# Optimization experiments

Measured on AMD Instinct MI355X. Metric: run time of the kernel, lower is better.

## Reference

```python
import jax, jax.numpy as jnp
import numpy as np

B, S, K, N, G = 2, 2048, 4096, 11008, 128  # tokens=B*S, group_size=G

def setup_inputs() -> dict:
    key = jax.random.key(0)
    k1, k2, k3, k4 = jax.random.split(key, 4)
    x = jax.random.normal(k1, (B, S, K), dtype=jnp.float16)
    # packed INT4 weights: one uint8 holds two nibbles along N (even col = low nibble)
    w_packed = jax.random.randint(k2, (K, N // 2), 0, 256, dtype=jnp.int32).astype(jnp.uint8)
    # realistic per-group scales (small positive) and integer zeros in [0,16)
    w_scale = (jax.random.uniform(k3, (K // G, N), dtype=jnp.float32) * 0.02 + 1e-3).astype(jnp.float16)
    w_zero = jax.random.randint(k4, (K // G, N), 0, 16).astype(jnp.float16)
    return {"x": x, "w_packed": w_packed, "w_scale": w_scale, "w_zero": w_zero}

def reference(x, w_packed, w_scale, w_zero):
    Kd, Nh = w_packed.shape  # [K, N//2]
    # unpack nibbles: even output column = low nibble, odd = high nibble
    low = (w_packed & 0xF).astype(jnp.float16)
    high = ((w_packed >> 4) & 0xF).astype(jnp.float16)
    w_int4 = jnp.stack([low, high], axis=-1).reshape(Kd, 2 * Nh)  # [K, N]
    # per-group dequant: group index = k // G along the K axis
    scale = jnp.repeat(w_scale, G, axis=0)  # [K, N]
    zero = jnp.repeat(w_zero, G, axis=0)    # [K, N]
    w = (w_int4 - zero) * scale             # fp16 dequantized weight [K, N]
    x2 = x.reshape(-1, Kd)                  # [M, K]
    # fp16 inputs, fp32 accumulation (matches tl.dot acc fp32), store fp16
    acc = jnp.einsum('mk,kn->mn', x2, w, preferred_element_type=jnp.float32)
    out = acc.astype(jnp.float16)
    return out.reshape(*x.shape[:-1], 2 * Nh)
```

## Files before the change

kernel.cpp:

```cpp
#include <hip/hip_runtime.h>
#include <hip/hip_bf16.h>
#include <stdint.h>

typedef __bf16 bf16_t;
typedef __bf16 bf16x8 __attribute__((ext_vector_type(8)));
typedef _Float16 f16;
typedef _Float16 f16x8 __attribute__((ext_vector_type(8)));
typedef _Float16 h2 __attribute__((ext_vector_type(2)));
typedef float floatx4 __attribute__((ext_vector_type(4)));
typedef uint32_t u32;

#define M_DIM 4096
#define K_DIM 4096
#define N_DIM 11008
#define GRP 128
#define NHALF (N_DIM / 2)
#define N64T (N_DIM / 64)
#define KTN (K_DIM / 64)
#define WB_DWORDS (N64T * KTN * 64 * 8)
#define WB_BYTES ((size_t)WB_DWORDS * 4)

__global__ __launch_bounds__(256) void repack_w_kernel(const int* __restrict__ wp,
                                                       u32* __restrict__ WB) {
  __shared__ unsigned char Wt[64][36];

  const u32 tid = threadIdx.x;
  const u32 n64 = blockIdx.x;
  const u32 kt  = blockIdx.y;

  {
    const u32 r = tid >> 2;
    const u32 c = (tid & 3u) * 8u;
    const int* src = wp + (size_t)(kt * 64u + r) * NHALF + n64 * 32u + c;
    int4 a = *(const int4*)(src);
    int4 b = *(const int4*)(src + 4);
    u32 lo = ((u32)a.x & 0xFFu) | (((u32)a.y & 0xFFu) << 8) |
             (((u32)a.z & 0xFFu) << 16) | (((u32)a.w & 0xFFu) << 24);
    u32 hi = ((u32)b.x & 0xFFu) | (((u32)b.y & 0xFFu) << 8) |
             (((u32)b.z & 0xFFu) << 16) | (((u32)b.w & 0xFFu) << 24);
    *(u32*)&Wt[r][c]      = lo;
    *(u32*)&Wt[r][c + 4u] = hi;
  }
  __syncthreads();

  const u32 tt    = tid & 3u;
  const u32 ks    = (tid >> 2) & 1u;
  const u32 lane0 = tid >> 3;
  const u32 l15   = lane0 & 15u;
  const u32 cb    = tt * 8u + (l15 >> 1);
  const u32 sh    = (l15 & 1u) * 4u;
  const size_t obase = ((size_t)(n64 * 64u + kt) * 64u) * 8u;

#pragma unroll
  for (int half = 0; half < 2; ++half) {
    const u32 lane = lane0 + (u32)half * 32u;
    const u32 kb   = ks * 32u + (lane >> 4) * 8u;
    u32 d = 0;
#pragma unroll
    for (int p = 0; p < 8; ++p) {
      const int j = (p < 4) ? (2 * p) : (2 * (p - 4) + 1);
      u32 byte = Wt[kb + (u32)j][cb];
      d |= ((byte >> sh) & 0xFu) << (4 * p);
    }
    WB[obase + tid + (u32)half * 256u] = d;
  }
}

__global__ __launch_bounds__(256) void gemm_int4_kernel(const float* __restrict__ x,
                                                        const u32* __restrict__ WB,
                                                        const float* __restrict__ wscale,
                                                        const float* __restrict__ wzero,
                                                        float* __restrict__ out) {
  __shared__ __align__(16) f16 As[128 * 64];

  const u32 tid  = threadIdx.x;
  const u32 lane = tid & 63u;
  const u32 wave = tid >> 6;
  const u32 l15  = lane & 15u;
  const u32 quad = lane >> 4;
  const u32 wr   = wave >> 1;
  const u32 wc   = wave & 1u;

  const u32 n0 = blockIdx.x * 128u;
  const u32 m0 = blockIdx.y * 128u;

  const u32 srow  = tid >> 3;
  const u32 sslot = tid & 7u;
  const float* xsrc = x + (size_t)(m0 + srow) * K_DIM + sslot * 8u;
  char* lds_dst = (char*)As + srow * 128u + ((sslot ^ (srow & 7u)) * 16u);

  const u32* wb_base = WB + ((size_t)((n0 >> 6) + wc) * KTN * 64u) * 8u + lane * 8u;

  const u32 arow = wr * 64u + l15;
  const f16* a0 = As + arow * 64u + (((quad)      ^ (l15 & 7u)) * 8u);
  const f16* a1 = As + arow * 64u + (((4u + quad) ^ (l15 & 7u)) * 8u);

  floatx4 acc[4][4];
  floatx4 zero4 = {0.f, 0.f, 0.f, 0.f};
#pragma unroll
  for (int i = 0; i < 4; ++i)
#pragma unroll
    for (int t = 0; t < 4; ++t) acc[i][t] = zero4;

  h2 s2[4], z2[4];
  const u32 nidx0 = n0 + wc * 64u + l15;

  for (u32 kt = 0; kt < KTN; ++kt) {
    const float* src = xsrc + kt * 64u;
    f16x8 av[4];
#pragma unroll
    for (int it = 0; it < 4; ++it) {
      float4 f0 = *(const float4*)(src + (size_t)it * 32 * K_DIM);
      float4 f1 = *(const float4*)(src + (size_t)it * 32 * K_DIM + 4);
      union { f16x8 v; h2 h[4]; } u;
      u.h[0] = __builtin_bit_cast(h2, __builtin_amdgcn_cvt_pkrtz(f0.x, f0.y));
      u.h[1] = __builtin_bit_cast(h2, __builtin_amdgcn_cvt_pkrtz(f0.z, f0.w));
      u.h[2] = __builtin_bit_cast(h2, __builtin_amdgcn_cvt_pkrtz(f1.x, f1.y));
      u.h[3] = __builtin_bit_cast(h2, __builtin_amdgcn_cvt_pkrtz(f1.z, f1.w));
      av[it] = u.v;
    }

    const u32* wp8 = wb_base + (size_t)kt * 512u;
    uint4 bq0 = *(const uint4*)(wp8);
    uint4 bq1 = *(const uint4*)(wp8 + 4u);

    if ((kt & 1u) == 0u) {
      const u32 g = kt >> 1;
#pragma unroll
      for (int t = 0; t < 4; ++t) {
        float s = wscale[g * N_DIM + nidx0 + (u32)t * 16u];
        float z = wzero [g * N_DIM + nidx0 + (u32)t * 16u];
        f16 sh_ = (f16)s;
        f16 zh_ = (f16)(1024.0f + z);
        h2 sv = {sh_, sh_};
        h2 zv = {zh_, zh_};
        s2[t] = sv;
        z2[t] = zv;
      }
    }

    __syncthreads();
#pragma unroll
    for (int it = 0; it < 4; ++it)
      *(f16x8*)(lds_dst + it * 4096) = av[it];
    __syncthreads();

#pragma unroll
    for (int ks = 0; ks < 2; ++ks) {
      f16x8 af[4];
      const f16* ab = ks ? a1 : a0;
#pragma unroll
      for (int i = 0; i < 4; ++i)
        af[i] = *(const f16x8*)(ab + i * 16 * 64);

      const uint4 bqv = ks ? bq1 : bq0;
      const u32 qs[4] = {bqv.x, bqv.y, bqv.z, bqv.w};
#pragma unroll
      for (int t = 0; t < 4; ++t) {
        const u32 q = qs[t];
        u32 w01 = (q & 0x000F000Fu) | 0x64006400u;
        u32 w23 = ((q >> 4) & 0x000F000Fu) | 0x64006400u;
        u32 w45 = ((q >> 8) & 0x000F000Fu) | 0x64006400u;
        u32 w67 = ((q >> 12) & 0x000F000Fu) | 0x64006400u;
        union { f16x8 v; h2 h[4]; } bf;
        bf.h[0] = (__builtin_bit_cast(h2, w01) - z2[t]) * s2[t];
        bf.h[1] = (__builtin_bit_cast(h2, w23) - z2[t]) * s2[t];
        bf.h[2] = (__builtin_bit_cast(h2, w45) - z2[t]) * s2[t];
        bf.h[3] = (__builtin_bit_cast(h2, w67) - z2[t]) * s2[t];
#pragma unroll
        for (int i = 0; i < 4; ++i)
          acc[i][t] = __builtin_amdgcn_mfma_f32_16x16x32_f16(af[i], bf.v, acc[i][t], 0, 0, 0);
      }
    }
  }

  const u32 col0 = n0 + wc * 64u + l15;
  const u32 row0 = m0 + wr * 64u + quad * 4u;
#pragma unroll
  for (int i = 0; i < 4; ++i)
#pragma unroll
    for (int t = 0; t < 4; ++t)
#pragma unroll
      for (int r = 0; r < 4; ++r)
        out[(size_t)(row0 + (u32)i * 16u + (u32)r) * N_DIM + col0 + (u32)t * 16u] =
            acc[i][t][r];
}

__global__ __launch_bounds__(256) void gemm_int4_direct(const float* __restrict__ x,
                                                        const int* __restrict__ wp,
                                                        const float* __restrict__ wscale,
                                                        const float* __restrict__ wzero,
                                                        float* __restrict__ out) {
  __shared__ __align__(16) bf16_t As[128 * 64];
  __shared__ unsigned char Wb[64 * 68];

  const u32 tid  = threadIdx.x;
  const u32 lane = tid & 63u;
  const u32 wave = tid >> 6;
  const u32 l15  = lane & 15u;
  const u32 quad = lane >> 4;

  const u32 n0 = blockIdx.x * 128u;
  const u32 m0 = blockIdx.y * 128u;

  const float* xsrc = x + (m0 + (tid >> 3)) * (u32)K_DIM + (tid & 7u) * 8u;
  char* lds_dst = (char*)(&As[0]) + tid * 16u;

  const u32 wrow = tid >> 2;
  const u32 wcol = (tid & 3u) * 16;
  const int* wsrc = wp + (size_t)wrow * NHALF + (n0 >> 1) + wcol;

  const u32 n_idx = n0 + wave * 32u + l15;
  const u32 bcol0 = (wave * 32u + l15) >> 1;
  const u32 bcol1 = (wave * 32u + 16u + l15) >> 1;
  const u32 nsh   = (l15 & 1u) * 4u;

  floatx4 acc[8][2];
  floatx4 zero4 = {0.f, 0.f, 0.f, 0.f};
#pragma unroll
  for (int i = 0; i < 8; ++i)
#pragma unroll
    for (int t = 0; t < 2; ++t) acc[i][t] = zero4;

  const bf16_t* afrag_base = &As[0] + l15 * 64u + quad * 8u;
  float sc[2], zs[2];

  for (u32 kt = 0; kt < K_DIM / 64u; ++kt) {
    const float* src = xsrc + kt * 64u;
    bf16x8 av[4];
#pragma unroll
    for (int it = 0; it < 4; ++it) {
      float4 f0 = *(const float4*)(src + it * 32 * K_DIM);
      float4 f1 = *(const float4*)(src + it * 32 * K_DIM + 4);
      bf16x8 v;
      v[0] = (bf16_t)f0.x; v[1] = (bf16_t)f0.y; v[2] = (bf16_t)f0.z; v[3] = (bf16_t)f0.w;
      v[4] = (bf16_t)f1.x; v[5] = (bf16_t)f1.y; v[6] = (bf16_t)f1.z; v[7] = (bf16_t)f1.w;
      av[it] = v;
    }

    const int* wsk = wsrc + (size_t)kt * 64u * NHALF;
    int4 wv[4];
#pragma unroll
    for (int q = 0; q < 4; ++q) wv[q] = *(const int4*)(wsk + q * 4);

    if ((kt & 1u) == 0u) {
      const u32 g = kt >> 1;
#pragma unroll
      for (int t = 0; t < 2; ++t) {
        float s = wscale[g * N_DIM + n_idx + t * 16u];
        float z = wzero[g * N_DIM + n_idx + t * 16u];
        sc[t] = s;
        zs[t] = s * z;
      }
    }

    __syncthreads();
#pragma unroll
    for (int it = 0; it < 4; ++it)
      *(bf16x8*)(lds_dst + it * 4096) = av[it];
#pragma unroll
    for (int q = 0; q < 4; ++q) {
      u32 d = ((u32)wv[q].x & 0xFFu) | (((u32)wv[q].y & 0xFFu) << 8) |
              (((u32)wv[q].z & 0xFFu) << 16) | (((u32)wv[q].w & 0xFFu) << 24);
      *(u32*)(&Wb[wrow * 68u + wcol + q * 4u]) = d;
    }
    __syncthreads();

#pragma unroll
    for (int ks = 0; ks < 2; ++ks) {
      bf16x8 af[8];
#pragma unroll
      for (int i = 0; i < 8; ++i)
        af[i] = *(const bf16x8*)(afrag_base + i * 16 * 64 + ks * 32);
#pragma unroll
      for (int t = 0; t < 2; ++t) {
        const u32 bc = t ? bcol1 : bcol0;
        bf16x8 bfr;
#pragma unroll
        for (int j = 0; j < 8; ++j) {
          u32 byte = Wb[(ks * 32u + quad * 8u + j) * 68u + bc];
          float w = (float)((byte >> nsh) & 0xFu) * sc[t] - zs[t];
          bfr[j] = (bf16_t)w;
        }
#pragma unroll
        for (int i = 0; i < 8; ++i)
          acc[i][t] = __builtin_amdgcn_mfma_f32_16x16x32_bf16(af[i], bfr, acc[i][t], 0, 0, 0);
      }
    }
  }

  const u32 col0 = n0 + wave * 32u + l15;
  const u32 row0 = m0 + quad * 4u;
#pragma unroll
  for (int i = 0; i < 8; ++i)
#pragma unroll
    for (int t = 0; t < 2; ++t)
#pragma unroll
      for (int r = 0; r < 4; ++r)
        out[(row0 + i * 16u + r) * (u32)N_DIM + col0 + t * 16u] = acc[i][t][r];
}

extern "C" void kernel_launch(void* const* d_in, const int* in_sizes, int n_in,
                              void* d_out, int out_size, void* d_ws, size_t ws_size,
                              hipStream_t stream) {
  const float* x      = (const float*)d_in[0];
  const int*   wp     = (const int*)d_in[1];
  const float* wscale = (const float*)d_in[2];
  const float* wzero  = (const float*)d_in[3];
  float*       out    = (float*)d_out;

  if (ws_size >= WB_BYTES && d_ws != nullptr) {
    u32* WB = (u32*)d_ws;
    repack_w_kernel<<<dim3(N64T, KTN), 256, 0, stream>>>(wp, WB);
    gemm_int4_kernel<<<dim3(N_DIM / 128, M_DIM / 128), 256, 0, stream>>>(x, WB, wscale, wzero, out);
  } else {
    gemm_int4_direct<<<dim3(N_DIM / 128, M_DIM / 128), 256, 0, stream>>>(x, wp, wscale, wzero, out);
  }
}
```

Measured before the change: 702.0 us.

## Double-buffer A tile in LDS, prefetch next tile, and remap workgroups per XCD

Restructures the GEMM main loop to use two LDS buffers for the A tile. Global loads of x, packed weights and scales for the next k-step are issued before the current tile's MFMA work, which cuts the loop to one barrier per step. It also launches a 1D grid and remaps block IDs so that each XCD gets a contiguous chunk of tiles sharing the same N column, aiming for better L2 reuse. In exchange the kernel uses twice the LDS and holds more registers for prefetched data, which may lower occupancy.

```diff
diff --git a/kernel.cpp b/kernel.cpp
--- a/kernel.cpp
+++ b/kernel.cpp
@@ -19,6 +19,8 @@
 #define KTN (K_DIM / 64)
 #define WB_DWORDS (N64T * KTN * 64 * 8)
 #define WB_BYTES ((size_t)WB_DWORDS * 4)
+#define NWG ((N_DIM / 128) * (M_DIM / 128))
+#define WG_PER_XCD (NWG / 8)
 
 __global__ __launch_bounds__(256) void repack_w_kernel(const int* __restrict__ wp,
                                                        u32* __restrict__ WB) {
@@ -66,12 +68,12 @@
   }
 }
 
-__global__ __launch_bounds__(256) void gemm_int4_kernel(const float* __restrict__ x,
-                                                        const u32* __restrict__ WB,
-                                                        const float* __restrict__ wscale,
-                                                        const float* __restrict__ wzero,
-                                                        float* __restrict__ out) {
-  __shared__ __align__(16) f16 As[128 * 64];
+__global__ __launch_bounds__(256) void gemm_int4_f16(const float* __restrict__ x,
+                                                     const u32* __restrict__ WB,
+                                                     const float* __restrict__ wscale,
+                                                     const float* __restrict__ wzero,
+                                                     float* __restrict__ out) {
+  __shared__ __align__(16) f16 As[2 * 128 * 64];
 
   const u32 tid  = threadIdx.x;
   const u32 lane = tid & 63u;
@@ -81,8 +83,10 @@
   const u32 wr   = wave >> 1;
   const u32 wc   = wave & 1u;
 
-  const u32 n0 = blockIdx.x * 128u;
-  const u32 m0 = blockIdx.y * 128u;
+  const u32 wgid = blockIdx.x;
+  const u32 gid  = (wgid & 7u) * WG_PER_XCD + (wgid >> 3);
+  const u32 n0   = (gid >> 5) * 128u;
+  const u32 m0   = (gid & 31u) * 128u;
 
   const u32 srow  = tid >> 3;
   const u32 sslot = tid & 7u;
@@ -91,9 +95,9 @@
 
   const u32* wb_base = WB + ((size_t)((n0 >> 6) + wc) * KTN * 64u) * 8u + lane * 8u;
 
-  const u32 arow = wr * 64u + l15;
-  const f16* a0 = As + arow * 64u + (((quad)      ^ (l15 & 7u)) * 8u);
-  const f16* a1 = As + arow * 64u + (((4u + quad) ^ (l15 & 7u)) * 8u);
+  const u32 abase = (wr * 64u + l15) * 64u;
+  const u32 sw0   = ((quad)      ^ (l15 & 7u)) * 8u;
+  const u32 sw1   = ((4u + quad) ^ (l15 & 7u)) * 8u;
 
   floatx4 acc[4][4];
   floatx4 zero4 = {0.f, 0.f, 0.f, 0.f};
@@ -102,58 +106,44 @@
 #pragma unroll
     for (int t = 0; t < 4; ++t) acc[i][t] = zero4;
 
-  h2 s2[4], z2[4];
   const u32 nidx0 = n0 + wc * 64u + l15;
 
-  for (u32 kt = 0; kt < KTN; ++kt) {
-    const float* src = xsrc + kt * 64u;
-    f16x8 av[4];
+  f16x8 nx[4];
+  auto loadx = [&](u32 kt) {
+    const float* p = xsrc + (size_t)kt * 64u;
 #pragma unroll
     for (int it = 0; it < 4; ++it) {
-      float4 f0 = *(const float4*)(src + (size_t)it * 32 * K_DIM);
-      float4 f1 = *(const float4*)(src + (size_t)it * 32 * K_DIM + 4);
+      float4 f0 = *(const float4*)(p + (size_t)it * 32 * K_DIM);
+      float4 f1 = *(const float4*)(p + (size_t)it * 32 * K_DIM + 4);
       union { f16x8 v; h2 h[4]; } u;
       u.h[0] = __builtin_bit_cast(h2, __builtin_amdgcn_cvt_pkrtz(f0.x, f0.y));
       u.h[1] = __builtin_bit_cast(h2, __builtin_amdgcn_cvt_pkrtz(f0.z, f0.w));
       u.h[2] = __builtin_bit_cast(h2, __builtin_amdgcn_cvt_pkrtz(f1.x, f1.y));
       u.h[3] = __builtin_bit_cast(h2, __builtin_amdgcn_cvt_pkrtz(f1.z, f1.w));
-      av[it] = u.v;
-    }
-
-    const u32* wp8 = wb_base + (size_t)kt * 512u;
-    uint4 bq0 = *(const uint4*)(wp8);
-    uint4 bq1 = *(const uint4*)(wp8 + 4u);
-
-    if ((kt & 1u) == 0u) {
-      const u32 g = kt >> 1;
-#pragma unroll
-      for (int t = 0; t < 4; ++t) {
-        float s = wscale[g * N_DIM + nidx0 + (u32)t * 16u];
-        float z = wzero [g * N_DIM + nidx0 + (u32)t * 16u];
-        f16 sh_ = (f16)s;
-        f16 zh_ = (f16)(1024.0f + z);
-        h2 sv = {sh_, sh_};
-        h2 zv = {zh_, zh_};
-        s2[t] = sv;
-        z2[t] = zv;
-      }
-    }
-
-    __syncthreads();
-#pragma unroll
-    for (int it = 0; it < 4; ++it)
-      *(f16x8*)(lds_dst + it * 4096) = av[it];
-    __syncthreads();
-
+      nx[it] = u.v;
+    }
+  };
+
+  loadx(0);
+  uint4 nbq0 = *(const uint4*)(wb_base);
+  uint4 nbq1 = *(const uint4*)(wb_base + 4u);
+  float fs[4], fz[4];
+#pragma unroll
+  for (int t = 0; t < 4; ++t) {
+    fs[t] = wscale[nidx0 + (u32)t * 16u];
+    fz[t] = wzero [nidx0 + (u32)t * 16u];
+  }
+  h2 s2[4], z2[4];
+
+  auto compute = [&](const f16* abuf, const uint4 bqa, const uint4 bqb) {
 #pragma unroll
     for (int ks = 0; ks < 2; ++ks) {
       f16x8 af[4];
-      const f16* ab = ks ? a1 : a0;
+      const f16* ab = abuf + abase + (ks ? sw1 : sw0);
 #pragma unroll
       for (int i = 0; i < 4; ++i)
         af[i] = *(const f16x8*)(ab + i * 16 * 64);
-
-      const uint4 bqv = ks ? bq1 : bq0;
+      const uint4 bqv = ks ? bqb : bqa;
       const u32 qs[4] = {bqv.x, bqv.y, bqv.z, bqv.w};
 #pragma unroll
       for (int t = 0; t < 4; ++t) {
@@ -172,6 +162,57 @@
           acc[i][t] = __builtin_amdgcn_mfma_f32_16x16x32_f16(af[i], bf.v, acc[i][t], 0, 0, 0);
       }
     }
+  };
+
+  for (u32 kt2 = 0; kt2 < KTN / 2; ++kt2) {
+#pragma unroll
+    for (int t = 0; t < 4; ++t) {
+      f16 sh_ = (f16)fs[t];
+      f16 zh_ = (f16)(1024.0f + fz[t]);
+      h2 sv = {sh_, sh_};
+      h2 zv = {zh_, zh_};
+      s2[t] = sv;
+      z2[t] = zv;
+    }
+    {
+      *(f16x8*)(lds_dst)         = nx[0];
+      *(f16x8*)(lds_dst + 4096)  = nx[1];
+      *(f16x8*)(lds_dst + 8192)  = nx[2];
+      *(f16x8*)(lds_dst + 12288) = nx[3];
+      uint4 cb0 = nbq0, cb1 = nbq1;
+      __syncthreads();
+      loadx(2u * kt2 + 1u);
+      {
+        const u32* wpn = wb_base + (size_t)(2u * kt2 + 1u) * 512u;
+        nbq0 = *(const uint4*)(wpn);
+        nbq1 = *(const uint4*)(wpn + 4u);
+      }
+      if (kt2 + 1u < (u32)(KTN / 2)) {
+        const u32 gofs = (kt2 + 1u) * (u32)N_DIM + nidx0;
+#pragma unroll
+        for (int t = 0; t < 4; ++t) {
+          fs[t] = wscale[gofs + (u32)t * 16u];
+          fz[t] = wzero [gofs + (u32)t * 16u];
+        }
+      }
+      compute(As, cb0, cb1);
+    }
+
+    {
+      *(f16x8*)(lds_dst + 16384)         = nx[0];
+      *(f16x8*)(lds_dst + 16384 + 4096)  = nx[1];
+      *(f16x8*)(lds_dst + 16384 + 8192)  = nx[2];
+      *(f16x8*)(lds_dst + 16384 + 12288) = nx[3];
+      uint4 cb0 = nbq0, cb1 = nbq1;
+      __syncthreads();
+      if (kt2 < (u32)(KTN / 2 - 1)) {
+        loadx(2u * kt2 + 2u);
+        const u32* wpn = wb_base + (size_t)(2u * kt2 + 2u) * 512u;
+        nbq0 = *(const uint4*)(wpn);
+        nbq1 = *(const uint4*)(wpn + 4u);
+      }
+      compute(As + 8192, cb0, cb1);
+    }
   }
 
   const u32 col0 = n0 + wc * 64u + l15;
@@ -312,7 +353,7 @@
   if (ws_size >= WB_BYTES && d_ws != nullptr) {
     u32* WB = (u32*)d_ws;
     repack_w_kernel<<<dim3(N64T, KTN), 256, 0, stream>>>(wp, WB);
-    gemm_int4_kernel<<<dim3(N_DIM / 128, M_DIM / 128), 256, 0, stream>>>(x, WB, wscale, wzero, out);
+    gemm_int4_f16<<<NWG, 256, 0, stream>>>(x, WB, wscale, wzero, out);
   } else {
     gemm_int4_direct<<<dim3(N_DIM / 128, M_DIM / 128), 256, 0, stream>>>(x, wp, wscale, wzero, out);
   }
```

Result: slower. 1.026 ms (+46.1%).

## Split waves along N so each wave covers all 128 rows and 32 columns

Applied to the files above, without the earlier changes.

The 128x128 block is now divided among its four waves along N only, so each wave computes a 128x32 output strip instead of a 64x64 quadrant. Each lane dequantizes two weight columns per k-step instead of four, which removes the duplicate dequantization that two waves previously did for the same columns. The cost is that every wave reads all eight A fragments from LDS per k-substep instead of four, which doubles LDS read traffic. Accumulator count and MFMA count per wave stay the same.

```diff
diff --git a/kernel.cpp b/kernel.cpp
--- a/kernel.cpp
+++ b/kernel.cpp
@@ -66,11 +66,11 @@
   }
 }
 
-__global__ __launch_bounds__(256) void gemm_int4_kernel(const float* __restrict__ x,
-                                                        const u32* __restrict__ WB,
-                                                        const float* __restrict__ wscale,
-                                                        const float* __restrict__ wzero,
-                                                        float* __restrict__ out) {
+__global__ __launch_bounds__(256) void gemm_int4_f16(const float* __restrict__ x,
+                                                     const u32* __restrict__ WB,
+                                                     const float* __restrict__ wscale,
+                                                     const float* __restrict__ wzero,
+                                                     float* __restrict__ out) {
   __shared__ __align__(16) f16 As[128 * 64];
 
   const u32 tid  = threadIdx.x;
@@ -78,8 +78,6 @@
   const u32 wave = tid >> 6;
   const u32 l15  = lane & 15u;
   const u32 quad = lane >> 4;
-  const u32 wr   = wave >> 1;
-  const u32 wc   = wave & 1u;
 
   const u32 n0 = blockIdx.x * 128u;
   const u32 m0 = blockIdx.y * 128u;
@@ -89,25 +87,27 @@
   const float* xsrc = x + (size_t)(m0 + srow) * K_DIM + sslot * 8u;
   char* lds_dst = (char*)As + srow * 128u + ((sslot ^ (srow & 7u)) * 16u);
 
-  const u32* wb_base = WB + ((size_t)((n0 >> 6) + wc) * KTN * 64u) * 8u + lane * 8u;
-
-  const u32 arow = wr * 64u + l15;
-  const f16* a0 = As + arow * 64u + (((quad)      ^ (l15 & 7u)) * 8u);
-  const f16* a1 = As + arow * 64u + (((4u + quad) ^ (l15 & 7u)) * 8u);
-
-  floatx4 acc[4][4];
+  const u32* wb_lane = WB + ((size_t)((n0 >> 6) + (wave >> 1)) * KTN * 512u)
+                         + lane * 8u + (wave & 1u) * 2u;
+
+  const u32 sw0 = ((quad)      ^ (l15 & 7u)) * 8u;
+  const u32 sw1 = ((4u + quad) ^ (l15 & 7u)) * 8u;
+  const f16* a0 = As + l15 * 64u + sw0;
+  const f16* a1 = As + l15 * 64u + sw1;
+
+  floatx4 acc[8][2];
   floatx4 zero4 = {0.f, 0.f, 0.f, 0.f};
 #pragma unroll
-  for (int i = 0; i < 4; ++i)
-#pragma unroll
-    for (int t = 0; t < 4; ++t) acc[i][t] = zero4;
-
-  h2 s2[4], z2[4];
-  const u32 nidx0 = n0 + wc * 64u + l15;
+  for (int i = 0; i < 8; ++i)
+#pragma unroll
+    for (int t = 0; t < 2; ++t) acc[i][t] = zero4;
+
+  const u32 nidx0 = n0 + wave * 32u + l15;
+  h2 s2[2], z2[2];
 
   for (u32 kt = 0; kt < KTN; ++kt) {
     const float* src = xsrc + kt * 64u;
-    f16x8 av[4];
+    f16x8 nx[4];
 #pragma unroll
     for (int it = 0; it < 4; ++it) {
       float4 f0 = *(const float4*)(src + (size_t)it * 32 * K_DIM);
@@ -117,17 +117,17 @@
       u.h[1] = __builtin_bit_cast(h2, __builtin_amdgcn_cvt_pkrtz(f0.z, f0.w));
       u.h[2] = __builtin_bit_cast(h2, __builtin_amdgcn_cvt_pkrtz(f1.x, f1.y));
       u.h[3] = __builtin_bit_cast(h2, __builtin_amdgcn_cvt_pkrtz(f1.z, f1.w));
-      av[it] = u.v;
-    }
-
-    const u32* wp8 = wb_base + (size_t)kt * 512u;
-    uint4 bq0 = *(const uint4*)(wp8);
-    uint4 bq1 = *(const uint4*)(wp8 + 4u);
+      nx[it] = u.v;
+    }
+
+    const u32* wp8 = wb_lane + (size_t)kt * 512u;
+    uint2 bqa = *(const uint2*)(wp8);
+    uint2 bqb = *(const uint2*)(wp8 + 4u);
 
     if ((kt & 1u) == 0u) {
       const u32 g = kt >> 1;
 #pragma unroll
-      for (int t = 0; t < 4; ++t) {
+      for (int t = 0; t < 2; ++t) {
         float s = wscale[g * N_DIM + nidx0 + (u32)t * 16u];
         float z = wzero [g * N_DIM + nidx0 + (u32)t * 16u];
         f16 sh_ = (f16)s;
@@ -140,46 +140,47 @@
     }
 
     __syncthreads();
-#pragma unroll
-    for (int it = 0; it < 4; ++it)
-      *(f16x8*)(lds_dst + it * 4096) = av[it];
+    *(f16x8*)(lds_dst)         = nx[0];
+    *(f16x8*)(lds_dst + 4096)  = nx[1];
+    *(f16x8*)(lds_dst + 8192)  = nx[2];
+    *(f16x8*)(lds_dst + 12288) = nx[3];
     __syncthreads();
 
 #pragma unroll
     for (int ks = 0; ks < 2; ++ks) {
-      f16x8 af[4];
-      const f16* ab = ks ? a1 : a0;
-#pragma unroll
-      for (int i = 0; i < 4; ++i)
-        af[i] = *(const f16x8*)(ab + i * 16 * 64);
-
-      const uint4 bqv = ks ? bq1 : bq0;
-      const u32 qs[4] = {bqv.x, bqv.y, bqv.z, bqv.w};
-#pragma unroll
-      for (int t = 0; t < 4; ++t) {
-        const u32 q = qs[t];
+      const u32 qw0 = ks ? bqb.x : bqa.x;
+      const u32 qw1 = ks ? bqb.y : bqa.y;
+      f16x8 bf[2];
+#pragma unroll
+      for (int t = 0; t < 2; ++t) {
+        const u32 q = t ? qw1 : qw0;
         u32 w01 = (q & 0x000F000Fu) | 0x64006400u;
         u32 w23 = ((q >> 4) & 0x000F000Fu) | 0x64006400u;
         u32 w45 = ((q >> 8) & 0x000F000Fu) | 0x64006400u;
         u32 w67 = ((q >> 12) & 0x000F000Fu) | 0x64006400u;
-        union { f16x8 v; h2 h[4]; } bf;
-        bf.h[0] = (__builtin_bit_cast(h2, w01) - z2[t]) * s2[t];
-        bf.h[1] = (__builtin_bit_cast(h2, w23) - z2[t]) * s2[t];
-        bf.h[2] = (__builtin_bit_cast(h2, w45) - z2[t]) * s2[t];
-        bf.h[3] = (__builtin_bit_cast(h2, w67) - z2[t]) * s2[t];
-#pragma unroll
-        for (int i = 0; i < 4; ++i)
-          acc[i][t] = __builtin_amdgcn_mfma_f32_16x16x32_f16(af[i], bf.v, acc[i][t], 0, 0, 0);
-      }
-    }
-  }
-
-  const u32 col0 = n0 + wc * 64u + l15;
-  const u32 row0 = m0 + wr * 64u + quad * 4u;
-#pragma unroll
-  for (int i = 0; i < 4; ++i)
-#pragma unroll
-    for (int t = 0; t < 4; ++t)
+        union { f16x8 v; h2 h[4]; } b;
+        b.h[0] = (__builtin_bit_cast(h2, w01) - z2[t]) * s2[t];
+        b.h[1] = (__builtin_bit_cast(h2, w23) - z2[t]) * s2[t];
+        b.h[2] = (__builtin_bit_cast(h2, w45) - z2[t]) * s2[t];
+        b.h[3] = (__builtin_bit_cast(h2, w67) - z2[t]) * s2[t];
+        bf[t] = b.v;
+      }
+      const f16* ab = ks ? a1 : a0;
+#pragma unroll
+      for (int i = 0; i < 8; ++i) {
+        f16x8 af = *(const f16x8*)(ab + i * 16 * 64);
+        acc[i][0] = __builtin_amdgcn_mfma_f32_16x16x32_f16(af, bf[0], acc[i][0], 0, 0, 0);
+        acc[i][1] = __builtin_amdgcn_mfma_f32_16x16x32_f16(af, bf[1], acc[i][1], 0, 0, 0);
+      }
+    }
+  }
+
+  const u32 col0 = n0 + wave * 32u + l15;
+  const u32 row0 = m0 + quad * 4u;
+#pragma unroll
+  for (int i = 0; i < 8; ++i)
+#pragma unroll
+    for (int t = 0; t < 2; ++t)
 #pragma unroll
       for (int r = 0; r < 4; ++r)
         out[(size_t)(row0 + (u32)i * 16u + (u32)r) * N_DIM + col0 + (u32)t * 16u] =
@@ -312,7 +313,7 @@
   if (ws_size >= WB_BYTES && d_ws != nullptr) {
     u32* WB = (u32*)d_ws;
     repack_w_kernel<<<dim3(N64T, KTN), 256, 0, stream>>>(wp, WB);
-    gemm_int4_kernel<<<dim3(N_DIM / 128, M_DIM / 128), 256, 0, stream>>>(x, WB, wscale, wzero, out);
+    gemm_int4_f16<<<dim3(N_DIM / 128, M_DIM / 128), 256, 0, stream>>>(x, WB, wscale, wzero, out);
   } else {
     gemm_int4_direct<<<dim3(N_DIM / 128, M_DIM / 128), 256, 0, stream>>>(x, wp, wscale, wzero, out);
   }
```

Result: faster. 666.7 us (-5.0%).
